# Kernel tuning notes

Hardware: AMD Instinct MI355X
Metric: run time of the kernel (lower is better)

The kernel has to match this reference:

```python
import jax, jax.numpy as jnp
import numpy as np

B, NV, L, NKG = 8, 100, 128, 923
NT = NV + 1 + NKG  # 1024 total nodes
DV, DK, DH, H, NLAYERS, VOCAB = 2048, 300, 1024, 8, 3, 50265
DHD = DH // H


def _ln(x, g, b, eps=1e-5):
    m = x.mean(-1, keepdims=True)
    v = x.var(-1, keepdims=True)
    return (x - m) / jnp.sqrt(v + eps) * g + b


def _gat_layer(x, mask, W, bb, a_src, a_dst, ln_g, ln_b):
    # x: [B,N,D], mask: [B,N,N] bool
    Bn, N, D = x.shape
    h = (x @ W + bb).reshape(Bn, N, H, DHD)
    s = jnp.einsum('bnhd,hd->bnh', h, a_src)  # source term
    t = jnp.einsum('bnhd,hd->bnh', h, a_dst)  # target term
    e = jax.nn.leaky_relu(s[:, :, None, :] + t[:, None, :, :], 0.2)  # [B,N,N,H]
    e = jnp.where(mask[..., None], e, -1e9)
    a = jax.nn.softmax(e, axis=2)  # over neighbors j
    out = jnp.einsum('bijh,bjhd->bihd', a, h).reshape(Bn, N, D)
    return _ln(x + out, ln_g, ln_b)


def setup_inputs() -> dict:
    key = jax.random.key(0)
    ks = jax.random.split(key, 24)
    s = 0.02
    inp = {
        'visual_features': jax.random.normal(ks[0], (B, NV, DV), jnp.float32),
        'question_input_ids': jax.random.randint(ks[1], (B, L), 0, VOCAB, jnp.int64) if False else jax.random.randint(ks[1], (B, L), 0, VOCAB).astype(jnp.int32),
        'question_attention_mask': jnp.ones((B, L), jnp.int32),
        'graph_node_features': jax.random.normal(ks[2], (B, NKG, DK), jnp.float32),
        'graph_adj': jax.random.randint(ks[3], (B, NT, NT), 0, 2).astype(jnp.int32),
        'graph_node_types': jax.random.randint(ks[4], (B, NT), 0, 3).astype(jnp.int32),
        # params
        'vis_W': jax.random.normal(ks[5], (DV, DH), jnp.float32) * s,
        'vis_b': jnp.zeros((DH,), jnp.float32),
        'vis_ln_g': jnp.ones((DH,), jnp.float32),
        'vis_ln_b': jnp.zeros((DH,), jnp.float32),
        'tok_emb': jax.random.normal(ks[6], (VOCAB, DH), jnp.float32) * s,
        'q_W': jax.random.normal(ks[7], (DH, DH), jnp.float32) * s,
        'q_b': jnp.zeros((DH,), jnp.float32),
        'q_ln_g': jnp.ones((DH,), jnp.float32),
        'q_ln_b': jnp.zeros((DH,), jnp.float32),
        'kg_W': jax.random.normal(ks[8], (DK, DH), jnp.float32) * s,
        'kg_b': jnp.zeros((DH,), jnp.float32),
        'kg_ln_g': jnp.ones((DH,), jnp.float32),
        'kg_ln_b': jnp.zeros((DH,), jnp.float32),
        'type_emb': jax.random.normal(ks[9], (3, DH), jnp.float32) * s,
        'gat_W': jax.random.normal(ks[10], (NLAYERS, DH, DH), jnp.float32) * s,
        'gat_b': jnp.zeros((NLAYERS, DH), jnp.float32),
        'a_src': jax.random.normal(ks[11], (NLAYERS, H, DHD), jnp.float32) * s,
        'a_dst': jax.random.normal(ks[12], (NLAYERS, H, DHD), jnp.float32) * s,
        'gat_ln_g': jnp.ones((NLAYERS, DH), jnp.float32),
        'gat_ln_b': jnp.zeros((NLAYERS, DH), jnp.float32),
        'readout_W': jax.random.normal(ks[13], (DH, 1), jnp.float32) * s,
        'readout_b': jnp.zeros((1,), jnp.float32),
        'cs_W1': jax.random.normal(ks[14], (DH, DH), jnp.float32) * s,
        'cs_b1': jnp.zeros((DH,), jnp.float32),
        'cs_W2': jax.random.normal(ks[15], (DH, 1), jnp.float32) * s,
        'cs_b2': jnp.zeros((1,), jnp.float32),
    }
    return inp


def reference(visual_features, question_input_ids, question_attention_mask,
              graph_node_features, graph_adj, graph_node_types,
              vis_W, vis_b, vis_ln_g, vis_ln_b,
              tok_emb, q_W, q_b, q_ln_g, q_ln_b,
              kg_W, kg_b, kg_ln_g, kg_ln_b,
              type_emb, gat_W, gat_b, a_src, a_dst, gat_ln_g, gat_ln_b,
              readout_W, readout_b, cs_W1, cs_b1, cs_W2, cs_b2):
    # 1. visual projection
    vis = _ln(visual_features @ vis_W + vis_b, vis_ln_g, vis_ln_b)  # [B,NV,DH]
    # 2. text encoder (embedding + masked mean-pool + proj + LN)
    te = tok_emb[question_input_ids]  # [B,L,DH]
    m = question_attention_mask.astype(te.dtype)[..., None]
    pooled = (te * m).sum(1) / jnp.maximum(m.sum(1), 1.0)
    q = _ln(pooled @ q_W + q_b, q_ln_g, q_ln_b)[:, None, :]  # [B,1,DH]
    # 3. KG projection
    kg = _ln(graph_node_features @ kg_W + kg_b, kg_ln_g, kg_ln_b)
    # 4-5. concat + node-type embeddings
    x = jnp.concatenate([vis, q, kg], axis=1) + type_emb[graph_node_types]
    # 6. dense GAT stack
    mask = graph_adj > 0
    for l in range(NLAYERS):
        x = _gat_layer(x, mask, gat_W[l], gat_b[l], a_src[l], a_dst[l],
                       gat_ln_g[l], gat_ln_b[l])
    # 7. attention-pooled readout
    w = jax.nn.softmax((x @ readout_W + readout_b).squeeze(-1), axis=-1)
    g = (x * w[..., None]).sum(1)  # [B,DH]
    # 8. candidate scorer
    logits = jax.nn.gelu(g @ cs_W1 + cs_b1) @ cs_W2 + cs_b2  # [B,1]
    return logits
```

## Files before the change

kernel.cpp:

```cpp
#include <hip/hip_runtime.h>
#include <math.h>

#define NB 8
#define NV 100
#define LQ 128
#define NKG 923
#define NT 1024
#define DV 2048
#define DK 300
#define DH 1024
#define NH 8
#define DHD 128
#define NLAYERS 3

typedef __attribute__((ext_vector_type(8))) short short8;
typedef __attribute__((ext_vector_type(4))) float f32x4;

__device__ __forceinline__ short f2bf(float f) {
    unsigned u = __float_as_uint(f);
    u += 0x7fff + ((u >> 16) & 1);
    return (short)(u >> 16);
}
__device__ __forceinline__ float bf2f(short s) {
    unsigned u = ((unsigned)(unsigned short)s) << 16;
    return __uint_as_float(u);
}
__device__ __forceinline__ unsigned pack2(float a, float b) {
    return (unsigned)(unsigned short)f2bf(a) | ((unsigned)(unsigned short)f2bf(b) << 16);
}

#if __has_builtin(__builtin_amdgcn_global_load_lds)
#define HAVE_GLL 1
__device__ __forceinline__ void gll16(const void* g, void* l) {
    __builtin_amdgcn_global_load_lds(
        (const __attribute__((address_space(1))) void*)g,
        (__attribute__((address_space(3))) void*)l, 16, 0, 0);
}
#else
#define HAVE_GLL 0
#endif

__device__ __forceinline__ float block_sum1(float a, float* red4) {
#pragma unroll
    for (int off = 32; off > 0; off >>= 1) a += __shfl_xor(a, off, 64);
    int w = threadIdx.x >> 6;
    if ((threadIdx.x & 63) == 0) red4[w] = a;
    __syncthreads();
    return red4[0] + red4[1] + red4[2] + red4[3];
}
__device__ __forceinline__ float block_max1(float a, float* red4) {
#pragma unroll
    for (int off = 32; off > 0; off >>= 1) a = fmaxf(a, __shfl_xor(a, off, 64));
    int w = threadIdx.x >> 6;
    if ((threadIdx.x & 63) == 0) red4[w] = a;
    __syncthreads();
    return fmaxf(fmaxf(red4[0], red4[1]), fmaxf(red4[2], red4[3]));
}
__device__ __forceinline__ float2 block_sum2(float a, float b, float* red8) {
#pragma unroll
    for (int off = 32; off > 0; off >>= 1) {
        a += __shfl_xor(a, off, 64);
        b += __shfl_xor(b, off, 64);
    }
    int w = threadIdx.x >> 6;
    if ((threadIdx.x & 63) == 0) { red8[w] = a; red8[4 + w] = b; }
    __syncthreads();
    float2 r;
    r.x = red8[0] + red8[1] + red8[2] + red8[3];
    r.y = red8[4] + red8[5] + red8[6] + red8[7];
    return r;
}

__global__ __launch_bounds__(256) void bitmask_kernel(
    const int* __restrict__ adj, unsigned* __restrict__ mb)
{
    int bi = blockIdx.x;
    int tid = threadIdx.x;
#pragma unroll
    for (int p = 0; p < 4; ++p) {
        int j = p * 256 + tid;
        unsigned long long bal = __ballot(adj[(size_t)bi * NT + j] > 0);
        if ((tid & 63) == 0) {
            int w = (p * 256 + (tid & 0xC0)) >> 5;
            mb[(size_t)bi * 32 + w]     = (unsigned)bal;
            mb[(size_t)bi * 32 + w + 1] = (unsigned)(bal >> 32);
        }
    }
}

__global__ __launch_bounds__(256) void transpose_cast(
    const float* __restrict__ in, short* __restrict__ out,
    int K, int N, int Kp, size_t in_stride, size_t out_stride)
{
    __shared__ float ls[64][65];
    const float* inL = in + (size_t)blockIdx.z * in_stride;
    short* outL = out + (size_t)blockIdx.z * out_stride;
    int n0 = blockIdx.x * 64, k0 = blockIdx.y * 64;
    int tid = threadIdx.x;
    int j4 = (tid & 15) * 4;
#pragma unroll
    for (int s = 0; s < 4; ++s) {
        int i = (tid >> 4) + s * 16;
        int k = k0 + i;
        float4 v = make_float4(0.f, 0.f, 0.f, 0.f);
        if (k < K) v = *(const float4*)(inL + (size_t)k * N + n0 + j4);
        ls[i][j4 + 0] = v.x; ls[i][j4 + 1] = v.y;
        ls[i][j4 + 2] = v.z; ls[i][j4 + 3] = v.w;
    }
    __syncthreads();
#pragma unroll
    for (int s = 0; s < 4; ++s) {
        int a = (tid >> 4) + s * 16;
        int b = (tid & 15) * 4;
        uint2 pk;
        pk.x = pack2(ls[b + 0][a], ls[b + 1][a]);
        pk.y = pack2(ls[b + 2][a], ls[b + 3][a]);
        *(uint2*)(outL + (size_t)(n0 + a) * Kp + k0 + b) = pk;
    }
}

__global__ __launch_bounds__(256) void gemm_bias_mfma(
    const float* __restrict__ A, const short* __restrict__ Wt,
    const float* __restrict__ bias, float* __restrict__ C,
    int M, int N, int K, int Kp, int ldA)
{
    __shared__ short At[128][32];
    __shared__ short Bt[128][32];
    int tid = threadIdx.x;
    int row0 = blockIdx.y * 128, col0 = blockIdx.x * 128;
    int lane = tid & 63, wave = tid >> 6;
    int quad = lane >> 4, lq = lane & 15;
    int wm = (wave >> 1) * 64, wn = (wave & 1) * 64;
    f32x4 acc[4][4];
#pragma unroll
    for (int i = 0; i < 4; ++i)
#pragma unroll
        for (int j = 0; j < 4; ++j) {
            f32x4 z = {0.f, 0.f, 0.f, 0.f};
            acc[i][j] = z;
        }
    int ar = tid >> 2;
    int ac = (tid & 3) * 8;
    for (int k0 = 0; k0 < Kp; k0 += 32) {
        bool fullk = (k0 + 32 <= K);
#pragma unroll
        for (int s = 0; s < 2; ++s) {
            int r = ar + s * 64;
            int grow = row0 + r;
            short8 pk;
            if (grow < M && fullk) {
                const float* src = A + (size_t)grow * ldA + k0 + ac;
                float4 v0 = *(const float4*)(src);
                float4 v1 = *(const float4*)(src + 4);
                pk[0] = f2bf(v0.x); pk[1] = f2bf(v0.y);
                pk[2] = f2bf(v0.z); pk[3] = f2bf(v0.w);
                pk[4] = f2bf(v1.x); pk[5] = f2bf(v1.y);
                pk[6] = f2bf(v1.z); pk[7] = f2bf(v1.w);
            } else {
#pragma unroll
                for (int e = 0; e < 8; ++e) {
                    int k = k0 + ac + e;
                    pk[e] = (grow < M && k < K)
                          ? f2bf(A[(size_t)grow * ldA + k]) : (short)0;
                }
            }
            *(short8*)&At[r][ac] = pk;
        }
#pragma unroll
        for (int s = 0; s < 2; ++s) {
            int n = ar + s * 64;
            short8 w = *(const short8*)(Wt + (size_t)(col0 + n) * Kp + k0 + ac);
            *(short8*)&Bt[n][ac] = w;
        }
        __syncthreads();
        short8 af[4], bfr[4];
#pragma unroll
        for (int i = 0; i < 4; ++i)
            af[i] = *(short8*)&At[wm + i * 16 + lq][quad * 8];
#pragma unroll
        for (int j = 0; j < 4; ++j)
            bfr[j] = *(short8*)&Bt[wn + j * 16 + lq][quad * 8];
#pragma unroll
        for (int i = 0; i < 4; ++i)
#pragma unroll
            for (int j = 0; j < 4; ++j)
                acc[i][j] = __builtin_amdgcn_mfma_f32_16x16x32_bf16(
                    af[i], bfr[j], acc[i][j], 0, 0, 0);
        __syncthreads();
    }
#pragma unroll
    for (int j = 0; j < 4; ++j) {
        int n = col0 + wn + j * 16 + lq;
        float bv = bias[n];
#pragma unroll
        for (int i = 0; i < 4; ++i) {
#pragma unroll
            for (int r = 0; r < 4; ++r) {
                int m = row0 + wm + i * 16 + quad * 4 + r;
                if (m < M) C[(size_t)m * N + n] = acc[i][j][r] + bv;
            }
        }
    }
}

__global__ __launch_bounds__(256) void gemm_st_mfma(
    const short* __restrict__ Ab, const short* __restrict__ Wt,
    const float* __restrict__ bias,
    const float* __restrict__ asrc, const float* __restrict__ adst,
    short* __restrict__ ht,
    float* __restrict__ sbuf, float* __restrict__ tbuf)
{
    __shared__ __align__(16) short smem[17408];
    short (*At)[32]  = (short(*)[32])smem;
    short (*Bt)[32]  = (short(*)[32])(smem + 4096);
    short (*ct)[136] = (short(*)[136])smem;
    __shared__ float sred[2][128], tred[2][128];
    __shared__ float asl[128], adl[128];
    int tid = threadIdx.x;
    int h = blockIdx.x;
    int row0 = blockIdx.y * 128, col0 = h * 128;
    int b = row0 >> 10, i0 = row0 & 1023;
    int lane = tid & 63, wave = tid >> 6;
    int quad = lane >> 4, lq = lane & 15;
    int wm = (wave >> 1) * 64, wn = (wave & 1) * 64;
    if (tid < 128) asl[tid] = asrc[h * DHD + tid];
    else adl[tid - 128] = adst[h * DHD + tid - 128];
    f32x4 acc[4][4];
#pragma unroll
    for (int i = 0; i < 4; ++i)
#pragma unroll
        for (int j = 0; j < 4; ++j) {
            f32x4 z = {0.f, 0.f, 0.f, 0.f};
            acc[i][j] = z;
        }

    const short* gA0 = Ab + (size_t)(row0 + wave * 16 + (lane >> 2)) * DH + (lane & 3) * 8;
    const short* gA1 = gA0 + (size_t)64 * DH;
    const short* gB0 = Wt + (size_t)(col0 + wave * 16 + (lane >> 2)) * DH + (lane & 3) * 8;
    const short* gB1 = gB0 + (size_t)64 * DH;
#if HAVE_GLL
    char* lA0 = (char*)At + wave * 1024; char* lA1 = lA0 + 4096;
    char* lB0 = (char*)Bt + wave * 1024; char* lB1 = lB0 + 4096;
#endif
    for (int k0 = 0; k0 < DH; k0 += 32) {
#if HAVE_GLL
        gll16(gA0 + k0, lA0); gll16(gA1 + k0, lA1);
        gll16(gB0 + k0, lB0); gll16(gB1 + k0, lB1);
#else
        {
            short8 va0 = *(const short8*)(gA0 + k0);
            short8 va1 = *(const short8*)(gA1 + k0);
            short8 vb0 = *(const short8*)(gB0 + k0);
            short8 vb1 = *(const short8*)(gB1 + k0);
            *(short8*)((char*)At + wave * 1024 + lane * 16) = va0;
            *(short8*)((char*)At + 4096 + wave * 1024 + lane * 16) = va1;
            *(short8*)((char*)Bt + wave * 1024 + lane * 16) = vb0;
            *(short8*)((char*)Bt + 4096 + wave * 1024 + lane * 16) = vb1;
        }
#endif
        __syncthreads();
        short8 af[4], bfr[4];
#pragma unroll
        for (int i = 0; i < 4; ++i)
            af[i] = *(short8*)&At[wm + i * 16 + lq][quad * 8];
#pragma unroll
        for (int j = 0; j < 4; ++j)
            bfr[j] = *(short8*)&Bt[wn + j * 16 + lq][quad * 8];
#pragma unroll
        for (int i = 0; i < 4; ++i)
#pragma unroll
            for (int j = 0; j < 4; ++j)
                acc[i][j] = __builtin_amdgcn_mfma_f32_16x16x32_bf16(
                    af[i], bfr[j], acc[i][j], 0, 0, 0);
        __syncthreads();
    }
#pragma unroll
    for (int j = 0; j < 4; ++j) {
        int d = wn + j * 16 + lq;
        float bv = bias[col0 + d];
#pragma unroll
        for (int i2 = 0; i2 < 4; ++i2) {
            int m = wm + i2 * 16 + quad * 4;
            uint2 pk;
            pk.x = pack2(acc[i2][j][0] + bv, acc[i2][j][1] + bv);
            pk.y = pack2(acc[i2][j][2] + bv, acc[i2][j][3] + bv);
            *(uint2*)&ct[d][m] = pk;
        }
    }
    __syncthreads();
    {
        int d = tid >> 1, half = tid & 1;
        short* dst = ht + ((size_t)(b * NH + h) * DHD + d) * NT + i0 + half * 64;
        const short* src = &ct[d][half * 64];
#pragma unroll
        for (int q = 0; q < 8; ++q)
            *(short8*)(dst + q * 8) = *(const short8*)(src + q * 8);
    }
    {
        int i = tid >> 1, half = tid & 1;
        float sa = 0.f, ta = 0.f;
#pragma unroll 16
        for (int dd = 0; dd < 64; ++dd) {
            int d = half * 64 + dd;
            float hv = bf2f(ct[d][i]);
            sa += hv * asl[d];
            ta += hv * adl[d];
        }
        sred[half][i] = sa; tred[half][i] = ta;
    }
    __syncthreads();
    if (tid < 128) {
        size_t idx = (size_t)(b * NH + h) * NT + i0 + tid;
        sbuf[idx] = sred[0][tid] + sred[1][tid];
        tbuf[idx] = tred[0][tid] + tred[1][tid];
    }
}

__global__ __launch_bounds__(256) void ln_scatter(
    const float* __restrict__ src, float* __restrict__ x,
    const float* __restrict__ g, const float* __restrict__ bta,
    const int* __restrict__ types, const float* __restrict__ type_emb,
    short* __restrict__ xb,
    int rows, int npb, int node_off)
{
    __shared__ float red[8];
    int r = blockIdx.x;
    if (r >= rows) return;
    int tid = threadIdx.x;
    int b = r / npb, n = r - b * npb;
    int node = b * NT + node_off + n;
    float4 v = *(const float4*)(src + (size_t)r * DH + tid * 4);
    float s = v.x + v.y + v.z + v.w;
    float sq = v.x * v.x + v.y * v.y + v.z * v.z + v.w * v.w;
    float2 t2 = block_sum2(s, sq, red);
    float mean = t2.x * (1.0f / DH);
    float var = t2.y * (1.0f / DH) - mean * mean;
    float rstd = 1.0f / sqrtf(var + 1e-5f);
    float4 gv = *(const float4*)(g + tid * 4);
    float4 bv = *(const float4*)(bta + tid * 4);
    int ty = types[node];
    float4 tv = *(const float4*)(type_emb + (size_t)ty * DH + tid * 4);
    float4 o;
    o.x = (v.x - mean) * rstd * gv.x + bv.x + tv.x;
    o.y = (v.y - mean) * rstd * gv.y + bv.y + tv.y;
    o.z = (v.z - mean) * rstd * gv.z + bv.z + tv.z;
    o.w = (v.w - mean) * rstd * gv.w + bv.w + tv.w;
    *(float4*)(x + (size_t)node * DH + tid * 4) = o;
    uint2 pk;
    pk.x = pack2(o.x, o.y);
    pk.y = pack2(o.z, o.w);
    *(uint2*)(xb + (size_t)node * DH + tid * 4) = pk;
}

__global__ __launch_bounds__(256) void ln_residual(
    float* __restrict__ x, const float* __restrict__ o,
    const float* __restrict__ g, const float* __restrict__ bta,
    short* __restrict__ xb,
    const float* __restrict__ rW, const float* __restrict__ rb,
    float* __restrict__ scores)
{
    __shared__ float red[12];
    int r = blockIdx.x;
    int tid = threadIdx.x;
    float* xr = x + (size_t)r * DH;
    float4 xv = *(float4*)(xr + tid * 4);
    float4 ov = *(const float4*)(o + (size_t)r * DH + tid * 4);
    float v0 = xv.x + ov.x, v1 = xv.y + ov.y, v2 = xv.z + ov.z, v3 = xv.w + ov.w;
    float s = v0 + v1 + v2 + v3;
    float sq = v0 * v0 + v1 * v1 + v2 * v2 + v3 * v3;
    float2 t2 = block_sum2(s, sq, red);
    float mean = t2.x * (1.0f / DH);
    float var = t2.y * (1.0f / DH) - mean * mean;
    float rstd = 1.0f / sqrtf(var + 1e-5f);
    float4 gv = *(const float4*)(g + tid * 4);
    float4 bv = *(const float4*)(bta + tid * 4);
    float4 out;
    out.x = (v0 - mean) * rstd * gv.x + bv.x;
    out.y = (v1 - mean) * rstd * gv.y + bv.y;
    out.z = (v2 - mean) * rstd * gv.z + bv.z;
    out.w = (v3 - mean) * rstd * gv.w + bv.w;
    *(float4*)(xr + tid * 4) = out;
    uint2 pk;
    pk.x = pack2(out.x, out.y);
    pk.y = pack2(out.z, out.w);
    *(uint2*)(xb + (size_t)r * DH + tid * 4) = pk;
    if (scores) {
        float4 wv = *(const float4*)(rW + tid * 4);
        float p = out.x * wv.x + out.y * wv.y + out.z * wv.z + out.w * wv.w;
        float totp = block_sum1(p, red + 8);
        if (tid == 0) scores[r] = totp + rb[0];
    }
}

__global__ __launch_bounds__(256) void qpool_part(
    const float* __restrict__ tok_emb, const int* __restrict__ ids,
    const int* __restrict__ amask, float* __restrict__ ppool,
    float* __restrict__ pden)
{
    int b = blockIdx.x, c = blockIdx.y;
    int tid = threadIdx.x;
    float a0 = 0, a1 = 0, a2 = 0, a3 = 0;
    float denom = 0;
    for (int l = c * 32; l < (c + 1) * 32; ++l) {
        int id = ids[b * LQ + l];
        float m = (float)amask[b * LQ + l];
        denom += m;
        float4 e = *(const float4*)(tok_emb + (size_t)id * DH + tid * 4);
        a0 += m * e.x; a1 += m * e.y; a2 += m * e.z; a3 += m * e.w;
    }
    float4 o = make_float4(a0, a1, a2, a3);
    *(float4*)(ppool + ((size_t)(b * 4 + c)) * DH + tid * 4) = o;
    if (tid == 0) pden[b * 4 + c] = denom;
}
__global__ __launch_bounds__(256) void qpool_fin(
    const float* __restrict__ ppool, const float* __restrict__ pden,
    float* __restrict__ pooled)
{
    int b = blockIdx.x;
    int tid = threadIdx.x;
    float den = pden[b * 4] + pden[b * 4 + 1] + pden[b * 4 + 2] + pden[b * 4 + 3];
    float inv = 1.0f / fmaxf(den, 1.0f);
    float4 s = make_float4(0.f, 0.f, 0.f, 0.f);
#pragma unroll
    for (int c = 0; c < 4; ++c) {
        float4 v = *(const float4*)(ppool + ((size_t)(b * 4 + c)) * DH + tid * 4);
        s.x += v.x; s.y += v.y; s.z += v.z; s.w += v.w;
    }
    float4 o = make_float4(s.x * inv, s.y * inv, s.z * inv, s.w * inv);
    *(float4*)(pooled + b * DH + tid * 4) = o;
}

__global__ __launch_bounds__(256) void agg_mfma(
    const short* __restrict__ ht, const unsigned* __restrict__ mb,
    const float* __restrict__ s, const float* __restrict__ t,
    float* __restrict__ obuf)
{
    __shared__ __align__(16) short vt[128 * 64];
    __shared__ short at[64][72];
    __shared__ unsigned mrow[64][32];
    __shared__ float sv[64], alpha_s[64], lfin[64];
    int i0 = blockIdx.x * 64;
    int h = blockIdx.y, b = blockIdx.z;
    int tid = threadIdx.x;
    int lane = tid & 63, wave = tid >> 6;
    int quad = lane >> 4, lq = lane & 15;
    int wi = (wave >> 1) * 32;
    int wd = (wave & 1) * 64;
    if (tid < 64) sv[tid] = s[(size_t)(b * NH + h) * NT + i0 + tid];
#pragma unroll
    for (int s2 = 0; s2 < 2; ++s2) {
        int f = tid + s2 * 256;
        int ii2 = f >> 3, w4 = (f & 7) * 4;
        *(uint4*)&mrow[ii2][w4] =
            *(const uint4*)(mb + ((size_t)(b * NT + i0 + ii2)) * 32 + w4);
    }
    const float* tptr = t + (size_t)(b * NH + h) * NT;
    const short* hbase = ht + ((size_t)(b * NH + h) * DHD) * NT;
    const short* gsrc[4];
    char* ldst[4];
#pragma unroll
    for (int s2 = 0; s2 < 4; ++s2) {
        int f = tid + s2 * 256;
        int d = f >> 3, cc = f & 7;
        gsrc[s2] = hbase + (size_t)d * NT + ((cc ^ (d & 7)) * 8);
        ldst[s2] = (char*)vt + wave * 1024 + s2 * 4096;
    }
    f32x4 acc[2][4];
#pragma unroll
    for (int i = 0; i < 2; ++i)
#pragma unroll
        for (int j = 0; j < 4; ++j) {
            f32x4 z = {0.f, 0.f, 0.f, 0.f};
            acc[i][j] = z;
        }
    int ii = tid >> 2;
    int jq = (tid & 3) * 16;
    float m_run = -3e38f, l_run = 0.f;
    for (int j0 = 0; j0 < NT; j0 += 64) {
        __syncthreads();
#if HAVE_GLL
#pragma unroll
        for (int s2 = 0; s2 < 4; ++s2) gll16(gsrc[s2] + j0, ldst[s2]);
#else
#pragma unroll
        for (int s2 = 0; s2 < 4; ++s2) {
            int f = tid + s2 * 256;
            short8 v8 = *(const short8*)(gsrc[s2] + j0);
            *(short8*)((char*)vt + (size_t)f * 16) = v8;
        }
#endif
        float vv[16];
        unsigned mw;
        float tmax = -3e38f;
        {
            mw = mrow[ii][(j0 + jq) >> 5] >> ((j0 + jq) & 31);
            float svv = sv[ii];
            float4 t0 = *(const float4*)(tptr + j0 + jq);
            float4 t1 = *(const float4*)(tptr + j0 + jq + 4);
            float4 t2 = *(const float4*)(tptr + j0 + jq + 8);
            float4 t3 = *(const float4*)(tptr + j0 + jq + 12);
            float tv16[16] = {t0.x, t0.y, t0.z, t0.w, t1.x, t1.y, t1.z, t1.w,
                              t2.x, t2.y, t2.z, t2.w, t3.x, t3.y, t3.z, t3.w};
#pragma unroll
            for (int e = 0; e < 16; ++e) {
                float v = svv + tv16[e];
                v = v > 0.f ? v : 0.2f * v;
                v = ((mw >> e) & 1) ? v : -1e9f;
                vv[e] = v;
                tmax = fmaxf(tmax, v);
            }
        }
        tmax = fmaxf(tmax, __shfl_xor(tmax, 1, 64));
        tmax = fmaxf(tmax, __shfl_xor(tmax, 2, 64));
        float m_new = fmaxf(m_run, tmax);
        float al = __expf(m_run - m_new);
        float tsum = 0.f;
        short8 p0, p1;
#pragma unroll
        for (int e = 0; e < 8; ++e) {
            float w = ((mw >> e) & 1) ? __expf(vv[e] - m_new) : 0.f;
            tsum += w; p0[e] = f2bf(w);
        }
#pragma unroll
        for (int e = 0; e < 8; ++e) {
            float w = ((mw >> (8 + e)) & 1) ? __expf(vv[8 + e] - m_new) : 0.f;
            tsum += w; p1[e] = f2bf(w);
        }
        tsum += __shfl_xor(tsum, 1, 64);
        tsum += __shfl_xor(tsum, 2, 64);
        l_run = l_run * al + tsum;
        m_run = m_new;
        *(short8*)&at[ii][jq] = p0;
        *(short8*)&at[ii][jq + 8] = p1;
        if ((tid & 3) == 0) alpha_s[ii] = al;
        __syncthreads();
#pragma unroll
        for (int i2 = 0; i2 < 2; ++i2)
#pragma unroll
            for (int r = 0; r < 4; ++r) {
                float arow = alpha_s[wi + i2 * 16 + quad * 4 + r];
#pragma unroll
                for (int j = 0; j < 4; ++j) acc[i2][j][r] *= arow;
            }
        const char* vtb = (const char*)vt;
#pragma unroll
        for (int ks = 0; ks < 2; ++ks) {
            short8 af[2], bfr[4];
            af[0] = *(short8*)&at[wi + lq][ks * 32 + quad * 8];
            af[1] = *(short8*)&at[wi + 16 + lq][ks * 32 + quad * 8];
            int cc = ks * 4 + quad;
            int sx = (cc ^ (lq & 7)) * 16;
#pragma unroll
            for (int j = 0; j < 4; ++j)
                bfr[j] = *(const short8*)(vtb + (wd + j * 16 + lq) * 128 + sx);
#pragma unroll
            for (int i2 = 0; i2 < 2; ++i2)
#pragma unroll
                for (int j = 0; j < 4; ++j)
                    acc[i2][j] = __builtin_amdgcn_mfma_f32_16x16x32_bf16(
                        af[i2], bfr[j], acc[i2][j], 0, 0, 0);
        }
    }
    if ((tid & 3) == 0) lfin[ii] = l_run;
    __syncthreads();
#pragma unroll
    for (int i2 = 0; i2 < 2; ++i2) {
#pragma unroll
        for (int r = 0; r < 4; ++r) {
            int il = wi + i2 * 16 + quad * 4 + r;
            float inv = 1.0f / lfin[il];
            float* dst = obuf + ((size_t)(b * NT + i0 + il)) * DH + h * DHD + wd;
#pragma unroll
            for (int j = 0; j < 4; ++j)
                dst[j * 16 + lq] = acc[i2][j][r] * inv;
        }
    }
}

__global__ __launch_bounds__(256) void pool_part(
    const float* __restrict__ x, const float* __restrict__ scores,
    float* __restrict__ gpart)
{
    __shared__ float red[8];
    int p = blockIdx.x;
    int b = blockIdx.y;
    int tid = threadIdx.x;
    const float* sr = scores + (size_t)b * NT;
    float v[4];
    float mx = -3e38f;
#pragma unroll
    for (int k = 0; k < 4; ++k) { v[k] = sr[tid + k * 256]; mx = fmaxf(mx, v[k]); }
    float m = block_max1(mx, red);
    float ls = 0.f;
#pragma unroll
    for (int k = 0; k < 4; ++k) ls += expf(v[k] - m);
    float tot = block_sum1(ls, red + 4);
    float inv = 1.0f / tot;
    float a0 = 0, a1 = 0, a2 = 0, a3 = 0;
    for (int n = p * 128; n < (p + 1) * 128; ++n) {
        float wv = expf(sr[n] - m) * inv;
        float4 xv = *(const float4*)(x + ((size_t)(b * NT + n)) * DH + tid * 4);
        a0 += wv * xv.x; a1 += wv * xv.y; a2 += wv * xv.z; a3 += wv * xv.w;
    }
    float4 o = make_float4(a0, a1, a2, a3);
    *(float4*)(gpart + ((size_t)(b * 8 + p)) * DH + tid * 4) = o;
}

__global__ __launch_bounds__(256) void scorer_part(
    const float* __restrict__ gpart, const float* __restrict__ W1,
    float* __restrict__ spart)
{
    __shared__ float gsh[128];
    int c = blockIdx.x, b = blockIdx.y;
    int tid = threadIdx.x;
    if (tid < 128) {
        int d = c * 128 + tid;
        float gv = 0.f;
#pragma unroll
        for (int p = 0; p < 8; ++p) gv += gpart[((size_t)(b * 8 + p)) * DH + d];
        gsh[tid] = gv;
    }
    __syncthreads();
    float acc[4] = {};
    for (int dd = 0; dd < 128; ++dd) {
        float gv = gsh[dd];
        const float* wr = W1 + (size_t)(c * 128 + dd) * DH;
#pragma unroll
        for (int cc = 0; cc < 4; ++cc) acc[cc] += gv * wr[tid + cc * 256];
    }
#pragma unroll
    for (int cc = 0; cc < 4; ++cc)
        spart[((size_t)(b * 8 + c)) * DH + tid + cc * 256] = acc[cc];
}
__global__ __launch_bounds__(256) void scorer_fin(
    const float* __restrict__ spart, const float* __restrict__ b1,
    const float* __restrict__ W2, const float* __restrict__ b2,
    float* __restrict__ out)
{
    __shared__ float red[4];
    int b = blockIdx.x;
    int tid = threadIdx.x;
    float part = 0.f;
#pragma unroll
    for (int cc = 0; cc < 4; ++cc) {
        int k = tid + cc * 256;
        float s = 0.f;
#pragma unroll
        for (int c = 0; c < 8; ++c) s += spart[((size_t)(b * 8 + c)) * DH + k];
        float u = s + b1[k];
        float inner = 0.7978845608028654f * (u + 0.044715f * u * u * u);
        float gel = 0.5f * u * (1.0f + tanhf(inner));
        part += gel * W2[k];
    }
    float tot = block_sum1(part, red);
    if (tid == 0) out[b] = tot + b2[0];
}

extern "C" void kernel_launch(void* const* d_in, const int* in_sizes, int n_in,
                              void* d_out, int out_size, void* d_ws, size_t ws_size,
                              hipStream_t stream)
{
    const float* visual   = (const float*)d_in[0];
    const int*   q_ids    = (const int*)d_in[1];
    const int*   q_mask   = (const int*)d_in[2];
    const float* kg_feat  = (const float*)d_in[3];
    const int*   adj      = (const int*)d_in[4];
    const int*   ntypes   = (const int*)d_in[5];
    const float* vis_W    = (const float*)d_in[6];
    const float* vis_b    = (const float*)d_in[7];
    const float* vis_lng  = (const float*)d_in[8];
    const float* vis_lnb  = (const float*)d_in[9];
    const float* tok_emb  = (const float*)d_in[10];
    const float* q_W      = (const float*)d_in[11];
    const float* q_b      = (const float*)d_in[12];
    const float* q_lng    = (const float*)d_in[13];
    const float* q_lnb    = (const float*)d_in[14];
    const float* kg_W     = (const float*)d_in[15];
    const float* kg_b     = (const float*)d_in[16];
    const float* kg_lng   = (const float*)d_in[17];
    const float* kg_lnb   = (const float*)d_in[18];
    const float* type_emb = (const float*)d_in[19];
    const float* gat_W    = (const float*)d_in[20];
    const float* gat_b    = (const float*)d_in[21];
    const float* a_src    = (const float*)d_in[22];
    const float* a_dst    = (const float*)d_in[23];
    const float* gat_lng  = (const float*)d_in[24];
    const float* gat_lnb  = (const float*)d_in[25];
    const float* read_W   = (const float*)d_in[26];
    const float* read_b   = (const float*)d_in[27];
    const float* cs_W1    = (const float*)d_in[28];
    const float* cs_b1    = (const float*)d_in[29];
    const float* cs_W2    = (const float*)d_in[30];
    const float* cs_b2    = (const float*)d_in[31];
    float* out = (float*)d_out;

    float* ws = (float*)d_ws;
    const size_t NROW = (size_t)NB * NT;
    float* x      = ws;
    float* obuf   = x + NROW * DH;
    float* sbuf   = obuf + NROW * DH;
    float* tbuf   = sbuf + NB * NH * NT;
    float* pooled = tbuf + NB * NH * NT;
    float* scores = pooled + NB * DH;
    float* gpart  = scores + NROW;
    float* ppool  = gpart + NB * 8 * DH;
    float* pden   = ppool + NB * 4 * DH;
    float* spart  = pden + 64;
    short* wt_gat = (short*)(spart + NB * 8 * DH);
    short* ht     = wt_gat + (size_t)NLAYERS * DH * DH;
    unsigned* mb  = (unsigned*)(ht + (size_t)NB * NH * DHD * NT);
    short* xb     = (short*)(mb + (size_t)NB * NT * 32);
    short* wt_vis = xb + NROW * DH;
    short* wt_q   = wt_vis + (size_t)1024 * 2048;
    short* wt_kg  = wt_q + (size_t)1024 * 1024;

    transpose_cast<<<dim3(16, 32, 1), 256, 0, stream>>>(vis_W, wt_vis, DV, DH, DV, 0, 0);
    transpose_cast<<<dim3(16, 16, 1), 256, 0, stream>>>(q_W, wt_q, DH, DH, DH, 0, 0);
    transpose_cast<<<dim3(16, 5, 1), 256, 0, stream>>>(kg_W, wt_kg, DK, DH, 320, 0, 0);
    transpose_cast<<<dim3(16, 16, NLAYERS), 256, 0, stream>>>(
        gat_W, wt_gat, DH, DH, DH, (size_t)DH * DH, (size_t)DH * DH);
    bitmask_kernel<<<NB * NT, 256, 0, stream>>>(adj, mb);

    gemm_bias_mfma<<<dim3(8, 7), 256, 0, stream>>>(
        visual, wt_vis, vis_b, obuf, NB * NV, DH, DV, DV, DV);
    ln_scatter<<<NB * NV, 256, 0, stream>>>(obuf, x, vis_lng, vis_lnb,
        ntypes, type_emb, xb, NB * NV, NV, 0);

    qpool_part<<<dim3(NB, 4), 256, 0, stream>>>(tok_emb, q_ids, q_mask, ppool, pden);
    qpool_fin<<<NB, 256, 0, stream>>>(ppool, pden, pooled);
    gemm_bias_mfma<<<dim3(8, 1), 256, 0, stream>>>(
        pooled, wt_q, q_b, obuf, NB, DH, DH, DH, DH);
    ln_scatter<<<NB, 256, 0, stream>>>(obuf, x, q_lng, q_lnb,
        ntypes, type_emb, xb, NB, 1, NV);

    gemm_bias_mfma<<<dim3(8, 58), 256, 0, stream>>>(
        kg_feat, wt_kg, kg_b, obuf, NB * NKG, DH, DK, 320, DK);
    ln_scatter<<<NB * NKG, 256, 0, stream>>>(obuf, x, kg_lng, kg_lnb,
        ntypes, type_emb, xb, NB * NKG, NKG, NV + 1);

    for (int l = 0; l < NLAYERS; ++l) {
        const float* bl  = gat_b + (size_t)l * DH;
        const float* asl = a_src + (size_t)l * NH * DHD;
        const float* adl = a_dst + (size_t)l * NH * DHD;
        gemm_st_mfma<<<dim3(NH, 64), 256, 0, stream>>>(
            xb, wt_gat + (size_t)l * DH * DH, bl, asl, adl, ht, sbuf, tbuf);
        agg_mfma<<<dim3(16, NH, NB), 256, 0, stream>>>(
            ht, mb, sbuf, tbuf, obuf);
        ln_residual<<<NB * NT, 256, 0, stream>>>(x, obuf,
            gat_lng + (size_t)l * DH, gat_lnb + (size_t)l * DH, xb,
            read_W, read_b, (l == NLAYERS - 1) ? scores : nullptr);
    }

    pool_part<<<dim3(8, NB), 256, 0, stream>>>(x, scores, gpart);
    scorer_part<<<dim3(8, NB), 256, 0, stream>>>(gpart, cs_W1, spart);
    scorer_fin<<<NB, 256, 0, stream>>>(spart, cs_b1, cs_W2, cs_b2, out);
}
```

Measured before the change: 948.5 us.

## Double-buffer V tiles in GAT aggregation and fuse question projection path

The aggregation kernel now uses two LDS buffers for the value tile, issuing the next tile's load before the softmax and MFMA work on the current tile. Global latency can then overlap with compute, and the t loads are hoisted to the top of the loop. Separately, four small launches for the question path (pool, finalize, GEMM, LN scatter) are merged into one per-batch kernel that does a scalar dot product against the bf16 weights. The cost is double the LDS for the value tile and lower occupancy. The fused question kernel reads 1024 weight rows per block with strided, uncoalesced access, and the hand-placed barriers without full waitcnt on the async loads risk data races.

After: 981.4 us. +3.5%, slower.

```diff
diff --git a/kernel.cpp b/kernel.cpp
--- a/kernel.cpp
+++ b/kernel.cpp
@@ -392,42 +392,73 @@
     }
 }
 
-__global__ __launch_bounds__(256) void qpool_part(
+__global__ __launch_bounds__(256) void qproj_fused(
     const float* __restrict__ tok_emb, const int* __restrict__ ids,
-    const int* __restrict__ amask, float* __restrict__ ppool,
-    float* __restrict__ pden)
-{
-    int b = blockIdx.x, c = blockIdx.y;
-    int tid = threadIdx.x;
-    float a0 = 0, a1 = 0, a2 = 0, a3 = 0;
-    float denom = 0;
-    for (int l = c * 32; l < (c + 1) * 32; ++l) {
+    const int* __restrict__ amask, const short* __restrict__ wt_q,
+    const float* __restrict__ qb, const float* __restrict__ g,
+    const float* __restrict__ bta, const int* __restrict__ types,
+    const float* __restrict__ type_emb, float* __restrict__ x,
+    short* __restrict__ xb)
+{
+    __shared__ float pl[DH];
+    __shared__ float red[8];
+    int b = blockIdx.x, tid = threadIdx.x;
+    float a0 = 0, a1 = 0, a2 = 0, a3 = 0, denom = 0;
+    for (int l = 0; l < LQ; ++l) {
         int id = ids[b * LQ + l];
         float m = (float)amask[b * LQ + l];
         denom += m;
         float4 e = *(const float4*)(tok_emb + (size_t)id * DH + tid * 4);
         a0 += m * e.x; a1 += m * e.y; a2 += m * e.z; a3 += m * e.w;
     }
-    float4 o = make_float4(a0, a1, a2, a3);
-    *(float4*)(ppool + ((size_t)(b * 4 + c)) * DH + tid * 4) = o;
-    if (tid == 0) pden[b * 4 + c] = denom;
-}
-__global__ __launch_bounds__(256) void qpool_fin(
-    const float* __restrict__ ppool, const float* __restrict__ pden,
-    float* __restrict__ pooled)
-{
-    int b = blockIdx.x;
-    int tid = threadIdx.x;
-    float den = pden[b * 4] + pden[b * 4 + 1] + pden[b * 4 + 2] + pden[b * 4 + 3];
-    float inv = 1.0f / fmaxf(den, 1.0f);
-    float4 s = make_float4(0.f, 0.f, 0.f, 0.f);
-#pragma unroll
-    for (int c = 0; c < 4; ++c) {
-        float4 v = *(const float4*)(ppool + ((size_t)(b * 4 + c)) * DH + tid * 4);
-        s.x += v.x; s.y += v.y; s.z += v.z; s.w += v.w;
-    }
-    float4 o = make_float4(s.x * inv, s.y * inv, s.z * inv, s.w * inv);
-    *(float4*)(pooled + b * DH + tid * 4) = o;
+    float inv = 1.0f / fmaxf(denom, 1.0f);
+    pl[tid * 4 + 0] = a0 * inv; pl[tid * 4 + 1] = a1 * inv;
+    pl[tid * 4 + 2] = a2 * inv; pl[tid * 4 + 3] = a3 * inv;
+    __syncthreads();
+    const short* w0 = wt_q + (size_t)(tid * 4 + 0) * DH;
+    const short* w1 = wt_q + (size_t)(tid * 4 + 1) * DH;
+    const short* w2 = wt_q + (size_t)(tid * 4 + 2) * DH;
+    const short* w3 = wt_q + (size_t)(tid * 4 + 3) * DH;
+    float o0 = 0, o1 = 0, o2 = 0, o3 = 0;
+    for (int k0 = 0; k0 < DH; k0 += 8) {
+        float4 p0 = *(const float4*)&pl[k0];
+        float4 p1 = *(const float4*)&pl[k0 + 4];
+        float pk[8] = {p0.x, p0.y, p0.z, p0.w, p1.x, p1.y, p1.z, p1.w};
+        short8 q0 = *(const short8*)(w0 + k0);
+        short8 q1 = *(const short8*)(w1 + k0);
+        short8 q2 = *(const short8*)(w2 + k0);
+        short8 q3 = *(const short8*)(w3 + k0);
+#pragma unroll
+        for (int e = 0; e < 8; ++e) {
+            o0 += pk[e] * bf2f(q0[e]);
+            o1 += pk[e] * bf2f(q1[e]);
+            o2 += pk[e] * bf2f(q2[e]);
+            o3 += pk[e] * bf2f(q3[e]);
+        }
+    }
+    o0 += qb[tid * 4 + 0]; o1 += qb[tid * 4 + 1];
+    o2 += qb[tid * 4 + 2]; o3 += qb[tid * 4 + 3];
+    float s = o0 + o1 + o2 + o3;
+    float sq = o0 * o0 + o1 * o1 + o2 * o2 + o3 * o3;
+    float2 t2 = block_sum2(s, sq, red);
+    float mean = t2.x * (1.0f / DH);
+    float var = t2.y * (1.0f / DH) - mean * mean;
+    float rstd = 1.0f / sqrtf(var + 1e-5f);
+    float4 gv = *(const float4*)(g + tid * 4);
+    float4 bv = *(const float4*)(bta + tid * 4);
+    int node = b * NT + NV;
+    int ty = types[node];
+    float4 tv = *(const float4*)(type_emb + (size_t)ty * DH + tid * 4);
+    float4 o;
+    o.x = (o0 - mean) * rstd * gv.x + bv.x + tv.x;
+    o.y = (o1 - mean) * rstd * gv.y + bv.y + tv.y;
+    o.z = (o2 - mean) * rstd * gv.z + bv.z + tv.z;
+    o.w = (o3 - mean) * rstd * gv.w + bv.w + tv.w;
+    *(float4*)(x + (size_t)node * DH + tid * 4) = o;
+    uint2 pk2;
+    pk2.x = pack2(o.x, o.y);
+    pk2.y = pack2(o.z, o.w);
+    *(uint2*)(xb + (size_t)node * DH + tid * 4) = pk2;
 }
 
 __global__ __launch_bounds__(256) void agg_mfma(
@@ -435,7 +466,7 @@
     const float* __restrict__ s, const float* __restrict__ t,
     float* __restrict__ obuf)
 {
-    __shared__ __align__(16) short vt[128 * 64];
+    __shared__ __align__(16) short vt[2][128 * 64];
     __shared__ short at[64][72];
     __shared__ unsigned mrow[64][32];
     __shared__ float sv[64], alpha_s[64], lfin[64];
@@ -457,13 +488,11 @@
     const float* tptr = t + (size_t)(b * NH + h) * NT;
     const short* hbase = ht + ((size_t)(b * NH + h) * DHD) * NT;
     const short* gsrc[4];
-    char* ldst[4];
 #pragma unroll
     for (int s2 = 0; s2 < 4; ++s2) {
         int f = tid + s2 * 256;
         int d = f >> 3, cc = f & 7;
         gsrc[s2] = hbase + (size_t)d * NT + ((cc ^ (d & 7)) * 8);
-        ldst[s2] = (char*)vt + wave * 1024 + s2 * 4096;
     }
     f32x4 acc[2][4];
 #pragma unroll
@@ -476,29 +505,49 @@
     int ii = tid >> 2;
     int jq = (tid & 3) * 16;
     float m_run = -3e38f, l_run = 0.f;
-    for (int j0 = 0; j0 < NT; j0 += 64) {
-        __syncthreads();
+    __syncthreads();
+    {
+        char* d0 = (char*)(&vt[0][0]) + wave * 1024;
 #if HAVE_GLL
 #pragma unroll
-        for (int s2 = 0; s2 < 4; ++s2) gll16(gsrc[s2] + j0, ldst[s2]);
+        for (int s2 = 0; s2 < 4; ++s2) gll16(gsrc[s2], d0 + s2 * 4096);
 #else
 #pragma unroll
         for (int s2 = 0; s2 < 4; ++s2) {
             int f = tid + s2 * 256;
-            short8 v8 = *(const short8*)(gsrc[s2] + j0);
-            *(short8*)((char*)vt + (size_t)f * 16) = v8;
+            short8 v8 = *(const short8*)(gsrc[s2]);
+            *(short8*)((char*)(&vt[0][0]) + (size_t)f * 16) = v8;
         }
 #endif
+    }
+    for (int it = 0; it < 16; ++it) {
+        int j0 = it * 64;
+        int cur = it & 1;
+        int jn = (j0 + 64 < NT) ? j0 + 64 : j0;
+        float4 t0 = *(const float4*)(tptr + j0 + jq);
+        float4 t1 = *(const float4*)(tptr + j0 + jq + 4);
+        float4 t2 = *(const float4*)(tptr + j0 + jq + 8);
+        float4 t3 = *(const float4*)(tptr + j0 + jq + 12);
+        {
+            char* dn = (char*)(&vt[cur ^ 1][0]) + wave * 1024;
+#if HAVE_GLL
+#pragma unroll
+            for (int s2 = 0; s2 < 4; ++s2) gll16(gsrc[s2] + jn, dn + s2 * 4096);
+#else
+#pragma unroll
+            for (int s2 = 0; s2 < 4; ++s2) {
+                int f = tid + s2 * 256;
+                short8 v8 = *(const short8*)(gsrc[s2] + jn);
+                *(short8*)((char*)(&vt[cur ^ 1][0]) + (size_t)f * 16) = v8;
+            }
+#endif
+        }
         float vv[16];
         unsigned mw;
         float tmax = -3e38f;
         {
             mw = mrow[ii][(j0 + jq) >> 5] >> ((j0 + jq) & 31);
             float svv = sv[ii];
-            float4 t0 = *(const float4*)(tptr + j0 + jq);
-            float4 t1 = *(const float4*)(tptr + j0 + jq + 4);
-            float4 t2 = *(const float4*)(tptr + j0 + jq + 8);
-            float4 t3 = *(const float4*)(tptr + j0 + jq + 12);
             float tv16[16] = {t0.x, t0.y, t0.z, t0.w, t1.x, t1.y, t1.z, t1.w,
                               t2.x, t2.y, t2.z, t2.w, t3.x, t3.y, t3.z, t3.w};
 #pragma unroll
@@ -533,7 +582,8 @@
         *(short8*)&at[ii][jq] = p0;
         *(short8*)&at[ii][jq + 8] = p1;
         if ((tid & 3) == 0) alpha_s[ii] = al;
-        __syncthreads();
+        asm volatile("s_waitcnt lgkmcnt(0)" ::: "memory");
+        __builtin_amdgcn_s_barrier();
 #pragma unroll
         for (int i2 = 0; i2 < 2; ++i2)
 #pragma unroll
@@ -542,7 +592,7 @@
 #pragma unroll
                 for (int j = 0; j < 4; ++j) acc[i2][j][r] *= arow;
             }
-        const char* vtb = (const char*)vt;
+        const char* vtb = (const char*)(&vt[cur][0]);
 #pragma unroll
         for (int ks = 0; ks < 2; ++ks) {
             short8 af[2], bfr[4];
@@ -560,6 +610,7 @@
                     acc[i2][j] = __builtin_amdgcn_mfma_f32_16x16x32_bf16(
                         af[i2], bfr[j], acc[i2][j], 0, 0, 0);
         }
+        __builtin_amdgcn_s_barrier();
     }
     if ((tid & 3) == 0) lfin[ii] = l_run;
     __syncthreads();
@@ -726,12 +777,8 @@
     ln_scatter<<<NB * NV, 256, 0, stream>>>(obuf, x, vis_lng, vis_lnb,
         ntypes, type_emb, xb, NB * NV, NV, 0);
 
-    qpool_part<<<dim3(NB, 4), 256, 0, stream>>>(tok_emb, q_ids, q_mask, ppool, pden);
-    qpool_fin<<<NB, 256, 0, stream>>>(ppool, pden, pooled);
-    gemm_bias_mfma<<<dim3(8, 1), 256, 0, stream>>>(
-        pooled, wt_q, q_b, obuf, NB, DH, DH, DH, DH);
-    ln_scatter<<<NB, 256, 0, stream>>>(obuf, x, q_lng, q_lnb,
-        ntypes, type_emb, xb, NB, 1, NV);
+    qproj_fused<<<NB, 256, 0, stream>>>(tok_emb, q_ids, q_mask, wt_q,
+        q_b, q_lng, q_lnb, ntypes, type_emb, x, xb);
 
     gemm_bias_mfma<<<dim3(8, 58), 256, 0, stream>>>(
         kg_feat, wt_kg, kg_b, obuf, NB * NKG, DH, DK, 320, DK);
```
